# Optimization experiments

Hardware: AMD Instinct MI355X
Metric: run time of the kernel (lower is better)

The kernel has to match this reference:

```python
import jax, jax.numpy as jnp
import numpy as np

N_NODES = 50000
NEG_SLOPE = 0.2


def gat_conv(x, W, att_src, att_dst, b, src, dst, n):
    # x: [N, F_in], W: [F_in, H*C], att_*: [H, C], b: [H*C]
    H, C = att_src.shape
    h = (x @ W).reshape(n, H, C)                       # [N, H, C]
    a_s = (h * att_src).sum(-1)                        # [N, H]
    a_d = (h * att_dst).sum(-1)                        # [N, H]
    e = jax.nn.leaky_relu(a_s[src] + a_d[dst], NEG_SLOPE)  # [E, H]
    # segment softmax over destination node (every node has a self-loop)
    m = jax.ops.segment_max(e, dst, num_segments=n)    # [N, H]
    ex = jnp.exp(e - m[dst])
    denom = jax.ops.segment_sum(ex, dst, num_segments=n)
    alpha = ex / denom[dst]                            # [E, H]
    out = jax.ops.segment_sum(alpha[:, :, None] * h[src], dst, num_segments=n)
    return out.reshape(n, H * C) + b


def setup_inputs() -> dict:
    key = jax.random.key(0)
    ks = jax.random.split(key, 10)
    n, e = N_NODES, 1600000
    x = jax.random.normal(ks[0], (n, 128), dtype=jnp.float32)
    edge_index = jax.random.randint(ks[1], (2, e), 0, n, dtype=jnp.int64)
    s = 0.1
    return {
        "x": x,
        "edge_index": edge_index,
        "W1": jax.random.normal(ks[2], (128, 128), dtype=jnp.float32) * s,
        "att_src1": jax.random.normal(ks[3], (4, 32), dtype=jnp.float32) * s,
        "att_dst1": jax.random.normal(ks[4], (4, 32), dtype=jnp.float32) * s,
        "b1": jnp.zeros((128,), dtype=jnp.float32),
        "W2": jax.random.normal(ks[5], (128, 128), dtype=jnp.float32) * s,
        "att_src2": jax.random.normal(ks[6], (4, 32), dtype=jnp.float32) * s,
        "att_dst2": jax.random.normal(ks[7], (4, 32), dtype=jnp.float32) * s,
        "b2": jnp.zeros((128,), dtype=jnp.float32),
    }


def reference(x, edge_index, W1, att_src1, att_dst1, b1, W2, att_src2, att_dst2, b2):
    n = x.shape[0]
    loops = jnp.arange(n, dtype=edge_index.dtype)
    src = jnp.concatenate([edge_index[0], loops])  # add self-loops (PyG default)
    dst = jnp.concatenate([edge_index[1], loops])
    h = gat_conv(x, W1, att_src1, att_dst1, b1, src, dst, n)
    h = jax.nn.relu(h)
    h = gat_conv(h, W2, att_src2, att_dst2, b2, src, dst, n)
    return (h, h)
```

## Files before the change

kernel.cpp:

```cpp
#include <hip/hip_runtime.h>
#include <hip/hip_bf16.h>
#include <hip/hip_fp16.h>


#define FDIM 128
#define NHEAD 4
#define NB 512

typedef __attribute__((ext_vector_type(16))) float f32x16;
typedef __attribute__((ext_vector_type(8)))  short s16x8;

__device__ inline unsigned short f2bf(float f) {
    union { float f; unsigned u; } v; v.f = f;
    unsigned r = v.u + 0x7fff + ((v.u >> 16) & 1);
    return (unsigned short)(r >> 16);
}
__device__ inline float2 bf2f(unsigned v) {
    union { unsigned u; float f; } a, b;
    a.u = v << 16;
    b.u = v & 0xffff0000u;
    return make_float2(a.f, b.f);
}
__device__ inline void splitbf(float f, short* hi, short* lo) {
    unsigned u = __float_as_uint(f);
    float rem = f - __uint_as_float(u & 0xffff0000u);
    *hi = (short)(u >> 16);
    *lo = (short)(__float_as_uint(rem) >> 16);
}

__global__ __launch_bounds__(256) void prep_hist(const float* __restrict__ W1,
                                                 short* __restrict__ B1hi,
                                                 short* __restrict__ B1lo,
                                                 const float* __restrict__ W2,
                                                 short* __restrict__ B2hi,
                                                 short* __restrict__ B2lo,
                                                 const int* __restrict__ dst, int E,
                                                 unsigned long long magic,
                                                 int* __restrict__ bcnt) {
    __shared__ int sh[NB];
    const int t = threadIdx.x;
    const int b = blockIdx.x;
    if (b < 128) {
        const float* W = (b < 64) ? W1 : W2;
        short* Bhi = (b < 64) ? B1hi : B2hi;
        short* Blo = (b < 64) ? B1lo : B2lo;
        int e = (b & 63) * 256 + t;
        int k = e >> 7, n = e & 127;
        short hi, lo;
        splitbf(W[e], &hi, &lo);
        int idx = n * 128 + (((k >> 3) ^ (n & 15)) << 3) + (k & 7);
        Bhi[idx] = hi;
        Blo[idx] = lo;
        return;
    }
    for (int i = t; i < NB; i += 256) sh[i] = 0;
    __syncthreads();
    const int stride = (gridDim.x - 128) * 256;
    for (int i = (b - 128) * 256 + t; i < E; i += stride) {
        int bk = (int)(((unsigned long long)(unsigned)dst[i] * magic) >> 40);
        atomicAdd(&sh[bk], 1);
    }
    __syncthreads();
    for (int i = t; i < NB; i += 256)
        if (sh[i]) atomicAdd(&bcnt[i], sh[i]);
}

__global__ __launch_bounds__(256) void gemm_mfma(const float* __restrict__ A,
                                                 const short* __restrict__ Bghi,
                                                 const short* __restrict__ Bglo,
                                                 unsigned short* __restrict__ H0,
                                                 unsigned short* __restrict__ H1,
                                                 const float* __restrict__ att_s,
                                                 const float* __restrict__ att_d,
                                                 float* __restrict__ a_s,
                                                 float* __restrict__ a_d, int M) {
    __shared__ short Bsm[2][16384];
    __shared__ float attsm[256];
    const int t = threadIdx.x;
    const int bm = blockIdx.x * 64;

    if (t < 128) attsm[t] = att_s[t];
    else         attsm[t] = att_d[t - 128];

    {
        const uint4* ghi = (const uint4*)Bghi;
        const uint4* glo = (const uint4*)Bglo;
        uint4* shi = (uint4*)&Bsm[0][0];
        uint4* slo = (uint4*)&Bsm[1][0];
        #pragma unroll
        for (int i = 0; i < 8; i++) {
            shi[t + i * 256] = ghi[t + i * 256];
            slo[t + i * 256] = glo[t + i * 256];
        }
    }

    const int lane = t & 63;
    const int w = t >> 6;
    const int wr = w >> 1, wc = w & 1;
    const int m  = lane & 31, h2 = lane >> 5;
    const int grow = bm + wr * 32 + m;

    s16x8 ahi[8], alo[8];
    {
        const bool ok = grow < M;
        const float* ap = A + (size_t)grow * 128 + 8 * h2;
        #pragma unroll
        for (int c = 0; c < 8; c++) {
            float ff[8];
            if (ok) {
                float4 f0 = *(const float4*)(ap + c * 16);
                float4 f1 = *(const float4*)(ap + c * 16 + 4);
                ff[0]=f0.x; ff[1]=f0.y; ff[2]=f0.z; ff[3]=f0.w;
                ff[4]=f1.x; ff[5]=f1.y; ff[6]=f1.z; ff[7]=f1.w;
            } else {
                #pragma unroll
                for (int j = 0; j < 8; j++) ff[j] = 0.f;
            }
            #pragma unroll
            for (int j = 0; j < 8; j++) {
                short hi, lo;
                splitbf(ff[j], &hi, &lo);
                ahi[c][j] = hi;
                alo[c][j] = lo;
            }
        }
    }
    __syncthreads();

    f32x16 acc[2];
    #pragma unroll
    for (int i = 0; i < 16; i++) { acc[0][i] = 0.f; acc[1][i] = 0.f; }

    #pragma unroll
    for (int ni = 0; ni < 2; ni++) {
        const int n = ni * 64 + wc * 32 + m;
        const int nbase = n * 128;
        #pragma unroll
        for (int c = 0; c < 8; c++) {
            int chunk8 = 2 * c + h2;
            int koff = ((chunk8 ^ (n & 15)) << 3);
            s16x8 bhi = *(const s16x8*)&Bsm[0][nbase + koff];
            s16x8 blo = *(const s16x8*)&Bsm[1][nbase + koff];
            acc[ni] = __builtin_amdgcn_mfma_f32_32x32x16_bf16(ahi[c], bhi, acc[ni], 0, 0, 0);
            acc[ni] = __builtin_amdgcn_mfma_f32_32x32x16_bf16(alo[c], bhi, acc[ni], 0, 0, 0);
            acc[ni] = __builtin_amdgcn_mfma_f32_32x32x16_bf16(ahi[c], blo, acc[ni], 0, 0, 0);
        }
    }

    __syncthreads();
    unsigned short* htile = (unsigned short*)&Bsm[0][0];
    #pragma unroll
    for (int ni = 0; ni < 2; ni++) {
        const int colg = ni * 64 + wc * 32 + m;
        #pragma unroll
        for (int r = 0; r < 16; r++) {
            int row = wr * 32 + (r & 3) + 8 * (r >> 2) + 4 * h2;
            htile[row * 128 + colg] = (short)f2bf(acc[ni][r]);
        }
    }
    __syncthreads();

    {
        const int r = t >> 2, q = t & 3;
        const int growr = bm + r;
        if (growr < M) {
            uint4 v0 = *(uint4*)&htile[r * 128 + q * 32];
            uint4 v1 = *(uint4*)&htile[r * 128 + q * 32 + 8];
            uint4 v2 = *(uint4*)&htile[r * 128 + q * 32 + 16];
            uint4 v3 = *(uint4*)&htile[r * 128 + q * 32 + 24];
            unsigned short* Hp = (q < 2) ? H0 : H1;
            uint4* hg = (uint4*)(Hp + (size_t)growr * 64);
            const int qq = q & 1;
            hg[qq * 4 + 0] = v0; hg[qq * 4 + 1] = v1;
            hg[qq * 4 + 2] = v2; hg[qq * 4 + 3] = v3;
            unsigned uu[16] = {v0.x, v0.y, v0.z, v0.w, v1.x, v1.y, v1.z, v1.w,
                               v2.x, v2.y, v2.z, v2.w, v3.x, v3.y, v3.z, v3.w};
            float ps = 0.f, pd = 0.f;
            #pragma unroll
            for (int i = 0; i < 16; i++) {
                float2 f = bf2f(uu[i]);
                ps += f.x * attsm[q * 32 + 2 * i]       + f.y * attsm[q * 32 + 2 * i + 1];
                pd += f.x * attsm[128 + q * 32 + 2 * i] + f.y * attsm[128 + q * 32 + 2 * i + 1];
            }
            a_s[growr * NHEAD + q] = ps;
            a_d[growr * NHEAD + q] = pd;
        }
    }
}

__global__ __launch_bounds__(256) void bucket_scan(const int* __restrict__ bcnt,
                                                   int* __restrict__ bbase,
                                                   int* __restrict__ bcursor,
                                                   int* __restrict__ row_ptr,
                                                   int N, int E) {
    __shared__ int wsum[4];
    const int t = threadIdx.x, lane = t & 63, wid = t >> 6;
    int v0 = bcnt[2 * t], v1 = bcnt[2 * t + 1];
    int s = v0 + v1, incl = s;
    #pragma unroll
    for (int o = 1; o < 64; o <<= 1) {
        int u = __shfl_up(incl, o, 64);
        if (lane >= o) incl += u;
    }
    if (lane == 63) wsum[wid] = incl;
    __syncthreads();
    if (t == 0) {
        int a = 0;
        #pragma unroll
        for (int i = 0; i < 4; i++) { int x = wsum[i]; wsum[i] = a; a += x; }
    }
    __syncthreads();
    int excl = wsum[wid] + incl - s;
    bbase[2 * t] = excl;          bcursor[2 * t] = excl;
    bbase[2 * t + 1] = excl + v0; bcursor[2 * t + 1] = excl + v0;
    if (t == 0) { bbase[NB] = E; row_ptr[N] = E; }
}

__global__ __launch_bounds__(256) void partition(const int* __restrict__ src,
                                                 const int* __restrict__ dst, int E,
                                                 unsigned long long magic,
                                                 int* __restrict__ bcursor,
                                                 int2* __restrict__ ebuf) {
    __shared__ int shc[NB];
    __shared__ int shb[NB];
    __shared__ int shcur[NB];
    const int t = threadIdx.x;
    for (int i = t; i < NB; i += 256) shc[i] = 0;
    __syncthreads();
    const int e0 = blockIdx.x * 4096;
    int myb[16], mys[16], myd[16];
    #pragma unroll
    for (int u = 0; u < 16; u++) {
        int i = e0 + u * 256 + t;
        if (i < E) {
            mys[u] = src[i];
            myd[u] = dst[i];
            int b = (int)(((unsigned long long)(unsigned)myd[u] * magic) >> 40);
            myb[u] = b;
            atomicAdd(&shc[b], 1);
        } else myb[u] = -1;
    }
    __syncthreads();
    for (int i = t; i < NB; i += 256) {
        int c = shc[i];
        shcur[i] = 0;
        if (c) shb[i] = atomicAdd(&bcursor[i], c);
    }
    __syncthreads();
    #pragma unroll
    for (int u = 0; u < 16; u++) {
        if (myb[u] >= 0) {
            int o = atomicAdd(&shcur[myb[u]], 1);
            ebuf[shb[myb[u]] + o] = make_int2(mys[u], myd[u]);
        }
    }
}

__global__ __launch_bounds__(256) void build_bucket(const int2* __restrict__ ebuf,
                                                    const int* __restrict__ bbase,
                                                    int npb, int N,
                                                    int* __restrict__ row_ptr,
                                                    int* __restrict__ col,
                                                    int* __restrict__ edst) {
    __shared__ int degl[256];
    __shared__ int curl[256];
    const int b = blockIdx.x;
    const int t = threadIdx.x, lane = t & 63, wid = t >> 6;
    const int base = bbase[b];
    const int cnt = bbase[b + 1] - base;
    const int node0 = b * npb;
    for (int i = t; i < npb; i += 256) degl[i] = 0;
    __syncthreads();
    for (int i = t; i < cnt; i += 256) {
        int d = ebuf[base + i].y;
        atomicAdd(&degl[d - node0], 1);
    }
    __syncthreads();
    if (wid == 0) {
        int run = 0;
        for (int c = 0; c * 64 < npb; c++) {
            int idx = c * 64 + lane;
            int v = (idx < npb) ? degl[idx] : 0;
            int incl = v;
            #pragma unroll
            for (int o = 1; o < 64; o <<= 1) {
                int u = __shfl_up(incl, o, 64);
                if (lane >= o) incl += u;
            }
            int excl = incl - v + run;
            if (idx < npb) {
                curl[idx] = excl;
                int node = node0 + idx;
                if (node < N) row_ptr[node] = base + excl;
            }
            run += __shfl(incl, 63, 64);
        }
    }
    __syncthreads();
    for (int i = t; i < cnt; i += 256) {
        int2 ed = ebuf[base + i];
        int p = atomicAdd(&curl[ed.y - node0], 1);
        col[base + p] = ed.x;
        edst[base + p] = ed.y;
    }
}

__global__ __launch_bounds__(256) void edge_w(const int* __restrict__ col,
                                              const int* __restrict__ edst,
                                              const float4* __restrict__ as4,
                                              const float4* __restrict__ ad4,
                                              int E,
                                              __half2* __restrict__ w0,
                                              __half2* __restrict__ w1) {
    int i = blockIdx.x * 256 + threadIdx.x;
    if (i >= E) return;
    float4 a = as4[col[i]];
    float4 b = ad4[edst[i]];
    float ex = a.x + b.x, ey = a.y + b.y, ez = a.z + b.z, ew = a.w + b.w;
    ex = fmaxf(ex, 0.2f * ex); ey = fmaxf(ey, 0.2f * ey);
    ez = fmaxf(ez, 0.2f * ez); ew = fmaxf(ew, 0.2f * ew);
    w0[i] = __floats2half2_rn(__expf(ex), __expf(ey));
    w1[i] = __floats2half2_rn(__expf(ez), __expf(ew));
}

__global__ __launch_bounds__(64) void aggregate(const unsigned* __restrict__ h0,
                                                const unsigned* __restrict__ h1,
                                                const __half2* __restrict__ w0,
                                                const __half2* __restrict__ w1,
                                                const float* __restrict__ a_s,
                                                const float* __restrict__ a_d,
                                                const int* __restrict__ row_ptr,
                                                const int* __restrict__ col,
                                                const float* __restrict__ bias,
                                                float* __restrict__ out,
                                                float* __restrict__ out2,
                                                int n, int do_relu) {
    const int b = blockIdx.x;
    const int p = b & 1;
    const unsigned* __restrict__ hp = p ? h1 : h0;
    const __half2* __restrict__ wp = p ? w1 : w0;
    const int t = threadIdx.x;
    const int g = t >> 5;
    const int li = t & 31;
    const int node = (b >> 1) * 2 + g;
    if (node >= n) return;
    const int hd = p * 2 + (li >> 4);
    const bool hiH = (li >> 4) != 0;

    float e = a_s[node * NHEAD + hd] + a_d[node * NHEAD + hd];
    e = fmaxf(e, 0.2f * e);
    float den = __expf(e);
    float2 hv = bf2f(hp[(size_t)node * 32 + li]);
    float num0 = den * hv.x, num1 = den * hv.y;

    const int beg = row_ptr[node], end = row_ptr[node + 1];
    int j = beg;
    for (; j + 8 <= end; j += 8) {
        int s[8];
        #pragma unroll
        for (int u = 0; u < 8; u++) s[u] = col[j + u];
        unsigned v[8]; __half2 hw[8];
        #pragma unroll
        for (int u = 0; u < 8; u++) v[u] = hp[(size_t)s[u] * 32 + li];
        #pragma unroll
        for (int u = 0; u < 8; u++) hw[u] = wp[j + u];
        #pragma unroll
        for (int u = 0; u < 8; u++) {
            float wgt = hiH ? __high2float(hw[u]) : __low2float(hw[u]);
            den += wgt;
            float2 f = bf2f(v[u]);
            num0 += wgt * f.x;
            num1 += wgt * f.y;
        }
    }
    for (; j < end; j++) {
        int s = col[j];
        __half2 hw = wp[j];
        float wgt = hiH ? __high2float(hw) : __low2float(hw);
        den += wgt;
        float2 f = bf2f(hp[(size_t)s * 32 + li]);
        num0 += wgt * f.x;
        num1 += wgt * f.y;
    }
    float2 bv = ((const float2*)bias)[p * 32 + li];
    float rd = 1.0f / den;
    float o0 = num0 * rd + bv.x;
    float o1 = num1 * rd + bv.y;
    if (do_relu) { o0 = fmaxf(o0, 0.f); o1 = fmaxf(o1, 0.f); }
    ((float2*)out)[(size_t)node * 64 + p * 32 + li] = make_float2(o0, o1);
    if (out2) ((float2*)out2)[(size_t)node * 64 + p * 32 + li] = make_float2(o0, o1);
}

extern "C" void kernel_launch(void* const* d_in, const int* in_sizes, int n_in,
                              void* d_out, int out_size, void* d_ws, size_t ws_size,
                              hipStream_t stream) {
    const float* x        = (const float*)d_in[0];
    const int*   edge     = (const int*)d_in[1];
    const float* W1       = (const float*)d_in[2];
    const float* att_s1   = (const float*)d_in[3];
    const float* att_d1   = (const float*)d_in[4];
    const float* b1       = (const float*)d_in[5];
    const float* W2       = (const float*)d_in[6];
    const float* att_s2   = (const float*)d_in[7];
    const float* att_d2   = (const float*)d_in[8];
    const float* b2       = (const float*)d_in[9];
    float* out = (float*)d_out;

    const int N = in_sizes[0] / FDIM;
    const int E = in_sizes[1] / 2;
    const int* src = edge;
    const int* dst = edge + E;

    const int npb = (N + NB - 1) / NB;
    const unsigned long long magic = ((1ull << 40) / (unsigned long long)npb) + 1;

    char* w = (char*)d_ws;
    size_t off = 0;
    auto alloc = [&](size_t bytes) { void* p = w + off; off = (off + bytes + 255) & ~(size_t)255; return p; };
    int*   row_ptr = (int*)alloc((size_t)(N + 1) * 4);
    int*   col     = (int*)alloc((size_t)E * 4);
    int*   edst    = (int*)alloc((size_t)E * 4);
    __half2* w0    = (__half2*)alloc((size_t)E * 4);
    __half2* w1    = (__half2*)alloc((size_t)E * 4);
    int*   bcnt    = (int*)alloc((size_t)NB * 4);
    int*   bbase   = (int*)alloc((size_t)(NB + 1) * 4);
    int*   bcursor = (int*)alloc((size_t)NB * 4);
    unsigned short* h0 = (unsigned short*)alloc((size_t)N * 64 * 2);
    unsigned short* h1 = (unsigned short*)alloc((size_t)N * 64 * 2);
    float* hx      = (float*)alloc((size_t)N * FDIM * 4);
    float* as1     = (float*)alloc((size_t)N * NHEAD * 4);
    float* ad1     = (float*)alloc((size_t)N * NHEAD * 4);
    float* as2     = (float*)alloc((size_t)N * NHEAD * 4);
    float* ad2     = (float*)alloc((size_t)N * NHEAD * 4);
    short* Bg1hi   = (short*)alloc((size_t)128 * 128 * 2);
    short* Bg1lo   = (short*)alloc((size_t)128 * 128 * 2);
    short* Bg2hi   = (short*)alloc((size_t)128 * 128 * 2);
    short* Bg2lo   = (short*)alloc((size_t)128 * 128 * 2);
    int2*  ebuf    = (int2*)hx;
    (void)ws_size;

    hipMemsetAsync(bcnt, 0, (size_t)NB * 4, stream);
    prep_hist<<<128 + 1024, 256, 0, stream>>>(W1, Bg1hi, Bg1lo, W2, Bg2hi, Bg2lo,
                                              dst, E, magic, bcnt);
    bucket_scan<<<1, 256, 0, stream>>>(bcnt, bbase, bcursor, row_ptr, N, E);
    partition<<<(E + 4095) / 4096, 256, 0, stream>>>(src, dst, E, magic, bcursor, ebuf);
    build_bucket<<<NB, 256, 0, stream>>>(ebuf, bbase, npb, N, row_ptr, col, edst);

    const int gblocks = (N + 63) / 64;
    const int eb = (E + 255) / 256;
    const int ablocks = ((N + 1) / 2) * 2;

    gemm_mfma<<<gblocks, 256, 0, stream>>>(x, Bg1hi, Bg1lo, h0, h1,
                                           att_s1, att_d1, as1, ad1, N);
    edge_w<<<eb, 256, 0, stream>>>(col, edst, (const float4*)as1, (const float4*)ad1,
                                   E, w0, w1);
    aggregate<<<ablocks, 64, 0, stream>>>((const unsigned*)h0, (const unsigned*)h1,
                                          w0, w1, as1, ad1, row_ptr, col, b1,
                                          hx, nullptr, N, 1);

    gemm_mfma<<<gblocks, 256, 0, stream>>>(hx, Bg2hi, Bg2lo, h0, h1,
                                           att_s2, att_d2, as2, ad2, N);
    edge_w<<<eb, 256, 0, stream>>>(col, edst, (const float4*)as2, (const float4*)ad2,
                                   E, w0, w1);
    aggregate<<<ablocks, 64, 0, stream>>>((const unsigned*)h0, (const unsigned*)h1,
                                          w0, w1, as2, ad2, row_ptr, col, b2,
                                          out, out + (size_t)N * FDIM, N, 0);
}
```

Before: 336.4 us.

## Split each node's edge list across four lane groups with prefetch and shuffle reduction

The aggregation kernel now gives each node a full 64-lane wavefront. Sixteen lanes cover one half-feature slice using 8-byte loads, and four groups of lanes take interleaved edges. Neighbor indices and weights for the next block of 16 edges are prefetched, and partial sums are combined with cross-group shuffles before a float4 store. This aims to shorten the serial per-node edge loop and widen memory accesses. The cost is the shuffle reduction plus padded dummy gathers for nodes whose degree is not a multiple of 16.

Result: slower. 345.6 us (+2.7%).

```diff
diff --git a/kernel.cpp b/kernel.cpp
--- a/kernel.cpp
+++ b/kernel.cpp
@@ -323,72 +323,109 @@
     w1[i] = __floats2half2_rn(__expf(ez), __expf(ew));
 }
 
-__global__ __launch_bounds__(64) void aggregate(const unsigned* __restrict__ h0,
-                                                const unsigned* __restrict__ h1,
-                                                const __half2* __restrict__ w0,
-                                                const __half2* __restrict__ w1,
-                                                const float* __restrict__ a_s,
-                                                const float* __restrict__ a_d,
-                                                const int* __restrict__ row_ptr,
-                                                const int* __restrict__ col,
-                                                const float* __restrict__ bias,
-                                                float* __restrict__ out,
-                                                float* __restrict__ out2,
-                                                int n, int do_relu) {
+__global__ __launch_bounds__(256) void aggregate(const unsigned* __restrict__ h0,
+                                                 const unsigned* __restrict__ h1,
+                                                 const __half2* __restrict__ w0,
+                                                 const __half2* __restrict__ w1,
+                                                 const float* __restrict__ a_s,
+                                                 const float* __restrict__ a_d,
+                                                 const int* __restrict__ row_ptr,
+                                                 const int* __restrict__ col,
+                                                 const float* __restrict__ bias,
+                                                 float* __restrict__ out,
+                                                 float* __restrict__ out2,
+                                                 int n, int do_relu) {
     const int b = blockIdx.x;
     const int p = b & 1;
     const unsigned* __restrict__ hp = p ? h1 : h0;
     const __half2* __restrict__ wp = p ? w1 : w0;
     const int t = threadIdx.x;
-    const int g = t >> 5;
-    const int li = t & 31;
-    const int node = (b >> 1) * 2 + g;
+    const int node = (b >> 1) * 4 + (t >> 6);
     if (node >= n) return;
-    const int hd = p * 2 + (li >> 4);
-    const bool hiH = (li >> 4) != 0;
-
-    float e = a_s[node * NHEAD + hd] + a_d[node * NHEAD + hd];
-    e = fmaxf(e, 0.2f * e);
-    float den = __expf(e);
-    float2 hv = bf2f(hp[(size_t)node * 32 + li]);
-    float num0 = den * hv.x, num1 = den * hv.y;
+    const int lane = t & 63;
+    const int g  = lane >> 4;
+    const int li = lane & 15;
+    const int hd = p * 2 + (li >> 3);
+    const bool hiH = (li >> 3) != 0;
+
+    float den = 0.f;
+    float nx0 = 0.f, ny0 = 0.f, nx1 = 0.f, ny1 = 0.f;
+    if (g == 0) {
+        float e = a_s[node * NHEAD + hd] + a_d[node * NHEAD + hd];
+        e = fmaxf(e, 0.2f * e);
+        den = __expf(e);
+        uint2 hv = *(const uint2*)&hp[(size_t)node * 32 + 2 * li];
+        float2 f0 = bf2f(hv.x), f1 = bf2f(hv.y);
+        nx0 = den * f0.x; ny0 = den * f0.y;
+        nx1 = den * f1.x; ny1 = den * f1.y;
+    }
 
     const int beg = row_ptr[node], end = row_ptr[node + 1];
-    int j = beg;
-    for (; j + 8 <= end; j += 8) {
-        int s[8];
-        #pragma unroll
-        for (int u = 0; u < 8; u++) s[u] = col[j + u];
-        unsigned v[8]; __half2 hw[8];
-        #pragma unroll
-        for (int u = 0; u < 8; u++) v[u] = hp[(size_t)s[u] * 32 + li];
-        #pragma unroll
-        for (int u = 0; u < 8; u++) hw[u] = wp[j + u];
-        #pragma unroll
-        for (int u = 0; u < 8; u++) {
-            float wgt = hiH ? __high2float(hw[u]) : __low2float(hw[u]);
+    const int nblk = (end - beg + 15) >> 4;
+
+    int cs[4]; unsigned cw[4];
+    #pragma unroll
+    for (int u = 0; u < 4; u++) {
+        int id = beg + u * 4 + g;
+        bool v = id < end;
+        cs[u] = v ? col[id] : node;
+        cw[u] = v ? *(const unsigned*)&wp[id] : 0u;
+    }
+
+    for (int blk = 0; blk < nblk; blk++) {
+        int ns[4]; unsigned nw[4];
+        const bool more = (blk + 1) < nblk;
+        if (more) {
+            int nbase = beg + (blk + 1) * 16;
+            #pragma unroll
+            for (int u = 0; u < 4; u++) {
+                int id = nbase + u * 4 + g;
+                bool v = id < end;
+                ns[u] = v ? col[id] : node;
+                nw[u] = v ? *(const unsigned*)&wp[id] : 0u;
+            }
+        }
+        uint2 hv[4];
+        #pragma unroll
+        for (int u = 0; u < 4; u++)
+            hv[u] = *(const uint2*)&hp[(size_t)cs[u] * 32 + 2 * li];
+        #pragma unroll
+        for (int u = 0; u < 4; u++) {
+            __half2 h2 = *(__half2*)&cw[u];
+            float wgt = hiH ? __high2float(h2) : __low2float(h2);
             den += wgt;
-            float2 f = bf2f(v[u]);
-            num0 += wgt * f.x;
-            num1 += wgt * f.y;
-        }
-    }
-    for (; j < end; j++) {
-        int s = col[j];
-        __half2 hw = wp[j];
-        float wgt = hiH ? __high2float(hw) : __low2float(hw);
-        den += wgt;
-        float2 f = bf2f(hp[(size_t)s * 32 + li]);
-        num0 += wgt * f.x;
-        num1 += wgt * f.y;
-    }
-    float2 bv = ((const float2*)bias)[p * 32 + li];
-    float rd = 1.0f / den;
-    float o0 = num0 * rd + bv.x;
-    float o1 = num1 * rd + bv.y;
-    if (do_relu) { o0 = fmaxf(o0, 0.f); o1 = fmaxf(o1, 0.f); }
-    ((float2*)out)[(size_t)node * 64 + p * 32 + li] = make_float2(o0, o1);
-    if (out2) ((float2*)out2)[(size_t)node * 64 + p * 32 + li] = make_float2(o0, o1);
+            float2 f0 = bf2f(hv[u].x), f1 = bf2f(hv[u].y);
+            nx0 += wgt * f0.x; ny0 += wgt * f0.y;
+            nx1 += wgt * f1.x; ny1 += wgt * f1.y;
+        }
+        if (more) {
+            #pragma unroll
+            for (int u = 0; u < 4; u++) { cs[u] = ns[u]; cw[u] = nw[u]; }
+        }
+    }
+
+    #pragma unroll
+    for (int off = 16; off < 64; off <<= 1) {
+        den += __shfl_xor(den, off, 64);
+        nx0 += __shfl_xor(nx0, off, 64);
+        ny0 += __shfl_xor(ny0, off, 64);
+        nx1 += __shfl_xor(nx1, off, 64);
+        ny1 += __shfl_xor(ny1, off, 64);
+    }
+
+    if (g == 0) {
+        float4 bv = ((const float4*)bias)[p * 16 + li];
+        float rd = 1.0f / den;
+        float4 o;
+        o.x = nx0 * rd + bv.x; o.y = ny0 * rd + bv.y;
+        o.z = nx1 * rd + bv.z; o.w = ny1 * rd + bv.w;
+        if (do_relu) {
+            o.x = fmaxf(o.x, 0.f); o.y = fmaxf(o.y, 0.f);
+            o.z = fmaxf(o.z, 0.f); o.w = fmaxf(o.w, 0.f);
+        }
+        ((float4*)out)[(size_t)node * 32 + p * 16 + li] = o;
+        if (out2) ((float4*)out2)[(size_t)node * 32 + p * 16 + li] = o;
+    }
 }
 
 extern "C" void kernel_launch(void* const* d_in, const int* in_sizes, int n_in,
@@ -448,21 +485,21 @@
 
     const int gblocks = (N + 63) / 64;
     const int eb = (E + 255) / 256;
-    const int ablocks = ((N + 1) / 2) * 2;
+    const int ablocks = ((N + 3) / 4) * 2;
 
     gemm_mfma<<<gblocks, 256, 0, stream>>>(x, Bg1hi, Bg1lo, h0, h1,
                                            att_s1, att_d1, as1, ad1, N);
     edge_w<<<eb, 256, 0, stream>>>(col, edst, (const float4*)as1, (const float4*)ad1,
                                    E, w0, w1);
-    aggregate<<<ablocks, 64, 0, stream>>>((const unsigned*)h0, (const unsigned*)h1,
-                                          w0, w1, as1, ad1, row_ptr, col, b1,
-                                          hx, nullptr, N, 1);
+    aggregate<<<ablocks, 256, 0, stream>>>((const unsigned*)h0, (const unsigned*)h1,
+                                           w0, w1, as1, ad1, row_ptr, col, b1,
+                                           hx, nullptr, N, 1);
 
     gemm_mfma<<<gblocks, 256, 0, stream>>>(hx, Bg2hi, Bg2lo, h0, h1,
                                            att_s2, att_d2, as2, ad2, N);
     edge_w<<<eb, 256, 0, stream>>>(col, edst, (const float4*)as2, (const float4*)ad2,
                                    E, w0, w1);
-    aggregate<<<ablocks, 64, 0, stream>>>((const unsigned*)h0, (const unsigned*)h1,
-                                          w0, w1, as2, ad2, row_ptr, col, b2,
-                                          out, out + (size_t)N * FDIM, N, 0);
-}
+    aggregate<<<ablocks, 256, 0, stream>>>((const unsigned*)h0, (const unsigned*)h1,
+                                           w0, w1, as2, ad2, row_ptr, col, b2,
+                                           out, out + (size_t)N * FDIM, N, 0);
+}
```

## Split features and edge weights into per-head planes for aggregation

Applied to the files above, without the earlier changes.

The bf16 feature matrix and fp16 edge weights are reorganised from two-head halves into four per-head planes. The aggregate kernel now assigns each block to one head, with 16 lanes per node and 4 nodes per block, so each gathered row segment is 64 bytes and each edge weight is a single half. Streaming loads and stores (col, weights, outputs) are marked nontemporal to reduce cache pollution. In exchange, the col and row_ptr traffic doubles because there are four head passes instead of two, and each gather segment is smaller, which could lower gather efficiency.

Result: slower. 426.4 us (+26.7%).

```diff
diff --git a/kernel.cpp b/kernel.cpp
--- a/kernel.cpp
+++ b/kernel.cpp
@@ -68,8 +68,7 @@
 __global__ __launch_bounds__(256) void gemm_mfma(const float* __restrict__ A,
                                                  const short* __restrict__ Bghi,
                                                  const short* __restrict__ Bglo,
-                                                 unsigned short* __restrict__ H0,
-                                                 unsigned short* __restrict__ H1,
+                                                 unsigned short* __restrict__ H,
                                                  const float* __restrict__ att_s,
                                                  const float* __restrict__ att_d,
                                                  float* __restrict__ a_s,
@@ -168,11 +167,8 @@
             uint4 v1 = *(uint4*)&htile[r * 128 + q * 32 + 8];
             uint4 v2 = *(uint4*)&htile[r * 128 + q * 32 + 16];
             uint4 v3 = *(uint4*)&htile[r * 128 + q * 32 + 24];
-            unsigned short* Hp = (q < 2) ? H0 : H1;
-            uint4* hg = (uint4*)(Hp + (size_t)growr * 64);
-            const int qq = q & 1;
-            hg[qq * 4 + 0] = v0; hg[qq * 4 + 1] = v1;
-            hg[qq * 4 + 2] = v2; hg[qq * 4 + 3] = v3;
+            uint4* hg = (uint4*)(H + ((size_t)q * M + growr) * 32);
+            hg[0] = v0; hg[1] = v1; hg[2] = v2; hg[3] = v3;
             unsigned uu[16] = {v0.x, v0.y, v0.z, v0.w, v1.x, v1.y, v1.z, v1.w,
                                v2.x, v2.y, v2.z, v2.w, v3.x, v3.y, v3.z, v3.w};
             float ps = 0.f, pd = 0.f;
@@ -310,8 +306,10 @@
                                               const float4* __restrict__ as4,
                                               const float4* __restrict__ ad4,
                                               int E,
-                                              __half2* __restrict__ w0,
-                                              __half2* __restrict__ w1) {
+                                              unsigned short* __restrict__ q0,
+                                              unsigned short* __restrict__ q1,
+                                              unsigned short* __restrict__ q2,
+                                              unsigned short* __restrict__ q3) {
     int i = blockIdx.x * 256 + threadIdx.x;
     if (i >= E) return;
     float4 a = as4[col[i]];
@@ -319,14 +317,18 @@
     float ex = a.x + b.x, ey = a.y + b.y, ez = a.z + b.z, ew = a.w + b.w;
     ex = fmaxf(ex, 0.2f * ex); ey = fmaxf(ey, 0.2f * ey);
     ez = fmaxf(ez, 0.2f * ez); ew = fmaxf(ew, 0.2f * ew);
-    w0[i] = __floats2half2_rn(__expf(ex), __expf(ey));
-    w1[i] = __floats2half2_rn(__expf(ez), __expf(ew));
-}
-
-__global__ __launch_bounds__(64) void aggregate(const unsigned* __restrict__ h0,
-                                                const unsigned* __restrict__ h1,
-                                                const __half2* __restrict__ w0,
-                                                const __half2* __restrict__ w1,
+    __half hx = __float2half(__expf(ex));
+    __half hy = __float2half(__expf(ey));
+    __half hz = __float2half(__expf(ez));
+    __half hw = __float2half(__expf(ew));
+    q0[i] = *(unsigned short*)&hx;
+    q1[i] = *(unsigned short*)&hy;
+    q2[i] = *(unsigned short*)&hz;
+    q3[i] = *(unsigned short*)&hw;
+}
+
+__global__ __launch_bounds__(64) void aggregate(const unsigned short* __restrict__ hq,
+                                                const unsigned short* __restrict__ wq,
                                                 const float* __restrict__ a_s,
                                                 const float* __restrict__ a_d,
                                                 const int* __restrict__ row_ptr,
@@ -334,39 +336,45 @@
                                                 const float* __restrict__ bias,
                                                 float* __restrict__ out,
                                                 float* __restrict__ out2,
-                                                int n, int do_relu) {
+                                                int n, int E, int do_relu) {
     const int b = blockIdx.x;
-    const int p = b & 1;
-    const unsigned* __restrict__ hp = p ? h1 : h0;
-    const __half2* __restrict__ wp = p ? w1 : w0;
+    const int p = b & 3;
+    const unsigned* __restrict__ hp =
+        (const unsigned*)(hq + (size_t)p * n * 32);
+    const unsigned short* __restrict__ wp = wq + (size_t)p * E;
     const int t = threadIdx.x;
-    const int g = t >> 5;
-    const int li = t & 31;
-    const int node = (b >> 1) * 2 + g;
-    if (node >= n) return;
-    const int hd = p * 2 + (li >> 4);
-    const bool hiH = (li >> 4) != 0;
-
-    float e = a_s[node * NHEAD + hd] + a_d[node * NHEAD + hd];
+    const int g  = t >> 4;
+    const int li = t & 15;
+    const int node = (b >> 2) * 4 + g;
+    const bool valid = node < n;
+    const int nd = valid ? node : 0;
+
+    float e = a_s[nd * NHEAD + p] + a_d[nd * NHEAD + p];
     e = fmaxf(e, 0.2f * e);
     float den = __expf(e);
-    float2 hv = bf2f(hp[(size_t)node * 32 + li]);
-    float num0 = den * hv.x, num1 = den * hv.y;
-
-    const int beg = row_ptr[node], end = row_ptr[node + 1];
+    float num0, num1;
+    {
+        float2 hv = bf2f(hp[(size_t)nd * 16 + li]);
+        num0 = den * hv.x;
+        num1 = den * hv.y;
+    }
+
+    const int beg = row_ptr[nd];
+    const int end = valid ? row_ptr[nd + 1] : beg;
     int j = beg;
     for (; j + 8 <= end; j += 8) {
         int s[8];
         #pragma unroll
-        for (int u = 0; u < 8; u++) s[u] = col[j + u];
-        unsigned v[8]; __half2 hw[8];
-        #pragma unroll
-        for (int u = 0; u < 8; u++) v[u] = hp[(size_t)s[u] * 32 + li];
-        #pragma unroll
-        for (int u = 0; u < 8; u++) hw[u] = wp[j + u];
+        for (int u = 0; u < 8; u++) s[u] = __builtin_nontemporal_load(&col[j + u]);
+        unsigned v[8];
+        #pragma unroll
+        for (int u = 0; u < 8; u++) v[u] = hp[(size_t)s[u] * 16 + li];
+        unsigned short hw[8];
+        #pragma unroll
+        for (int u = 0; u < 8; u++) hw[u] = __builtin_nontemporal_load(&wp[j + u]);
         #pragma unroll
         for (int u = 0; u < 8; u++) {
-            float wgt = hiH ? __high2float(hw[u]) : __low2float(hw[u]);
+            float wgt = __half2float(*(const __half*)&hw[u]);
             den += wgt;
             float2 f = bf2f(v[u]);
             num0 += wgt * f.x;
@@ -375,20 +383,27 @@
     }
     for (; j < end; j++) {
         int s = col[j];
-        __half2 hw = wp[j];
-        float wgt = hiH ? __high2float(hw) : __low2float(hw);
+        unsigned short hw = wp[j];
+        float wgt = __half2float(*(const __half*)&hw);
         den += wgt;
-        float2 f = bf2f(hp[(size_t)s * 32 + li]);
+        float2 f = bf2f(hp[(size_t)s * 16 + li]);
         num0 += wgt * f.x;
         num1 += wgt * f.y;
     }
-    float2 bv = ((const float2*)bias)[p * 32 + li];
-    float rd = 1.0f / den;
-    float o0 = num0 * rd + bv.x;
-    float o1 = num1 * rd + bv.y;
-    if (do_relu) { o0 = fmaxf(o0, 0.f); o1 = fmaxf(o1, 0.f); }
-    ((float2*)out)[(size_t)node * 64 + p * 32 + li] = make_float2(o0, o1);
-    if (out2) ((float2*)out2)[(size_t)node * 64 + p * 32 + li] = make_float2(o0, o1);
+
+    if (valid) {
+        float2 bv = ((const float2*)bias)[p * 16 + li];
+        float rd = 1.0f / den;
+        float o0 = num0 * rd + bv.x;
+        float o1 = num1 * rd + bv.y;
+        if (do_relu) { o0 = fmaxf(o0, 0.f); o1 = fmaxf(o1, 0.f); }
+        float2 o = make_float2(o0, o1);
+        double dv;
+        __builtin_memcpy(&dv, &o, 8);
+        __builtin_nontemporal_store(dv, (double*)((float2*)out + (size_t)node * 64 + p * 16 + li));
+        if (out2)
+            __builtin_nontemporal_store(dv, (double*)((float2*)out2 + (size_t)node * 64 + p * 16 + li));
+    }
 }
 
 extern "C" void kernel_launch(void* const* d_in, const int* in_sizes, int n_in,
@@ -420,13 +435,11 @@
     int*   row_ptr = (int*)alloc((size_t)(N + 1) * 4);
     int*   col     = (int*)alloc((size_t)E * 4);
     int*   edst    = (int*)alloc((size_t)E * 4);
-    __half2* w0    = (__half2*)alloc((size_t)E * 4);
-    __half2* w1    = (__half2*)alloc((size_t)E * 4);
+    unsigned short* wqa = (unsigned short*)alloc((size_t)4 * E * 2);
     int*   bcnt    = (int*)alloc((size_t)NB * 4);
     int*   bbase   = (int*)alloc((size_t)(NB + 1) * 4);
     int*   bcursor = (int*)alloc((size_t)NB * 4);
-    unsigned short* h0 = (unsigned short*)alloc((size_t)N * 64 * 2);
-    unsigned short* h1 = (unsigned short*)alloc((size_t)N * 64 * 2);
+    unsigned short* h = (unsigned short*)alloc((size_t)4 * N * 32 * 2);
     float* hx      = (float*)alloc((size_t)N * FDIM * 4);
     float* as1     = (float*)alloc((size_t)N * NHEAD * 4);
     float* ad1     = (float*)alloc((size_t)N * NHEAD * 4);
@@ -448,21 +461,21 @@
 
     const int gblocks = (N + 63) / 64;
     const int eb = (E + 255) / 256;
-    const int ablocks = ((N + 1) / 2) * 2;
-
-    gemm_mfma<<<gblocks, 256, 0, stream>>>(x, Bg1hi, Bg1lo, h0, h1,
+    const int ablocks = ((N + 3) / 4) * 4;
+
+    gemm_mfma<<<gblocks, 256, 0, stream>>>(x, Bg1hi, Bg1lo, h,
                                            att_s1, att_d1, as1, ad1, N);
     edge_w<<<eb, 256, 0, stream>>>(col, edst, (const float4*)as1, (const float4*)ad1,
-                                   E, w0, w1);
-    aggregate<<<ablocks, 64, 0, stream>>>((const unsigned*)h0, (const unsigned*)h1,
-                                          w0, w1, as1, ad1, row_ptr, col, b1,
-                                          hx, nullptr, N, 1);
-
-    gemm_mfma<<<gblocks, 256, 0, stream>>>(hx, Bg2hi, Bg2lo, h0, h1,
+                                   E, wqa, wqa + (size_t)E, wqa + (size_t)2 * E,
+                                   wqa + (size_t)3 * E);
+    aggregate<<<ablocks, 64, 0, stream>>>(h, wqa, as1, ad1, row_ptr, col, b1,
+                                          hx, nullptr, N, E, 1);
+
+    gemm_mfma<<<gblocks, 256, 0, stream>>>(hx, Bg2hi, Bg2lo, h,
                                            att_s2, att_d2, as2, ad2, N);
     edge_w<<<eb, 256, 0, stream>>>(col, edst, (const float4*)as2, (const float4*)ad2,
-                                   E, w0, w1);
-    aggregate<<<ablocks, 64, 0, stream>>>((const unsigned*)h0, (const unsigned*)h1,
-                                          w0, w1, as2, ad2, row_ptr, col, b2,
-                                          out, out + (size_t)N * FDIM, N, 0);
-}
+                                   E, wqa, wqa + (size_t)E, wqa + (size_t)2 * E,
+                                   wqa + (size_t)3 * E);
+    aggregate<<<ablocks, 64, 0, stream>>>(h, wqa, as2, ad2, row_ptr, col, b2,
+                                          out, out + (size_t)N * FDIM, N, E, 0);
+}
```

## Fuse edge attention weights into aggregate and store scores head-major

Applied to the files above, without the earlier changes.

Removes the separate edge_w kernel and the per-edge fp16 weight arrays and destination index array. The aggregate kernel now gathers the source attention score per edge and computes leaky-relu and exp inline. The a_s/a_d score arrays are switched to head-major layout so each half-wave gathers from a contiguous per-head array. This saves two edge-sized passes and their global writes and reads, at the cost of an extra random gather and an exp per edge inside aggregate. The gemm kernel must use M as the row count for the new layout.

Result: faster. 327.8 us (-2.6%).

```diff
diff --git a/kernel.cpp b/kernel.cpp
--- a/kernel.cpp
+++ b/kernel.cpp
@@ -182,8 +182,8 @@
                 ps += f.x * attsm[q * 32 + 2 * i]       + f.y * attsm[q * 32 + 2 * i + 1];
                 pd += f.x * attsm[128 + q * 32 + 2 * i] + f.y * attsm[128 + q * 32 + 2 * i + 1];
             }
-            a_s[growr * NHEAD + q] = ps;
-            a_d[growr * NHEAD + q] = pd;
+            a_s[(size_t)q * M + growr] = ps;
+            a_d[(size_t)q * M + growr] = pd;
         }
     }
 }
@@ -260,8 +260,7 @@
                                                     const int* __restrict__ bbase,
                                                     int npb, int N,
                                                     int* __restrict__ row_ptr,
-                                                    int* __restrict__ col,
-                                                    int* __restrict__ edst) {
+                                                    int* __restrict__ col) {
     __shared__ int degl[256];
     __shared__ int curl[256];
     const int b = blockIdx.x;
@@ -301,32 +300,11 @@
         int2 ed = ebuf[base + i];
         int p = atomicAdd(&curl[ed.y - node0], 1);
         col[base + p] = ed.x;
-        edst[base + p] = ed.y;
-    }
-}
-
-__global__ __launch_bounds__(256) void edge_w(const int* __restrict__ col,
-                                              const int* __restrict__ edst,
-                                              const float4* __restrict__ as4,
-                                              const float4* __restrict__ ad4,
-                                              int E,
-                                              __half2* __restrict__ w0,
-                                              __half2* __restrict__ w1) {
-    int i = blockIdx.x * 256 + threadIdx.x;
-    if (i >= E) return;
-    float4 a = as4[col[i]];
-    float4 b = ad4[edst[i]];
-    float ex = a.x + b.x, ey = a.y + b.y, ez = a.z + b.z, ew = a.w + b.w;
-    ex = fmaxf(ex, 0.2f * ex); ey = fmaxf(ey, 0.2f * ey);
-    ez = fmaxf(ez, 0.2f * ez); ew = fmaxf(ew, 0.2f * ew);
-    w0[i] = __floats2half2_rn(__expf(ex), __expf(ey));
-    w1[i] = __floats2half2_rn(__expf(ez), __expf(ew));
+    }
 }
 
 __global__ __launch_bounds__(64) void aggregate(const unsigned* __restrict__ h0,
                                                 const unsigned* __restrict__ h1,
-                                                const __half2* __restrict__ w0,
-                                                const __half2* __restrict__ w1,
                                                 const float* __restrict__ a_s,
                                                 const float* __restrict__ a_d,
                                                 const int* __restrict__ row_ptr,
@@ -338,16 +316,16 @@
     const int b = blockIdx.x;
     const int p = b & 1;
     const unsigned* __restrict__ hp = p ? h1 : h0;
-    const __half2* __restrict__ wp = p ? w1 : w0;
     const int t = threadIdx.x;
     const int g = t >> 5;
     const int li = t & 31;
     const int node = (b >> 1) * 2 + g;
     if (node >= n) return;
     const int hd = p * 2 + (li >> 4);
-    const bool hiH = (li >> 4) != 0;
-
-    float e = a_s[node * NHEAD + hd] + a_d[node * NHEAD + hd];
+    const float* __restrict__ as_h = a_s + (size_t)hd * n;
+    const float adv = a_d[(size_t)hd * n + node];
+
+    float e = as_h[node] + adv;
     e = fmaxf(e, 0.2f * e);
     float den = __expf(e);
     float2 hv = bf2f(hp[(size_t)node * 32 + li]);
@@ -359,14 +337,17 @@
         int s[8];
         #pragma unroll
         for (int u = 0; u < 8; u++) s[u] = col[j + u];
-        unsigned v[8]; __half2 hw[8];
+        unsigned v[8];
         #pragma unroll
         for (int u = 0; u < 8; u++) v[u] = hp[(size_t)s[u] * 32 + li];
-        #pragma unroll
-        for (int u = 0; u < 8; u++) hw[u] = wp[j + u];
+        float av[8];
+        #pragma unroll
+        for (int u = 0; u < 8; u++) av[u] = as_h[s[u]];
         #pragma unroll
         for (int u = 0; u < 8; u++) {
-            float wgt = hiH ? __high2float(hw[u]) : __low2float(hw[u]);
+            float ee = av[u] + adv;
+            ee = fmaxf(ee, 0.2f * ee);
+            float wgt = __expf(ee);
             den += wgt;
             float2 f = bf2f(v[u]);
             num0 += wgt * f.x;
@@ -375,8 +356,9 @@
     }
     for (; j < end; j++) {
         int s = col[j];
-        __half2 hw = wp[j];
-        float wgt = hiH ? __high2float(hw) : __low2float(hw);
+        float ee = as_h[s] + adv;
+        ee = fmaxf(ee, 0.2f * ee);
+        float wgt = __expf(ee);
         den += wgt;
         float2 f = bf2f(hp[(size_t)s * 32 + li]);
         num0 += wgt * f.x;
@@ -419,19 +401,16 @@
     auto alloc = [&](size_t bytes) { void* p = w + off; off = (off + bytes + 255) & ~(size_t)255; return p; };
     int*   row_ptr = (int*)alloc((size_t)(N + 1) * 4);
     int*   col     = (int*)alloc((size_t)E * 4);
-    int*   edst    = (int*)alloc((size_t)E * 4);
-    __half2* w0    = (__half2*)alloc((size_t)E * 4);
-    __half2* w1    = (__half2*)alloc((size_t)E * 4);
     int*   bcnt    = (int*)alloc((size_t)NB * 4);
     int*   bbase   = (int*)alloc((size_t)(NB + 1) * 4);
     int*   bcursor = (int*)alloc((size_t)NB * 4);
     unsigned short* h0 = (unsigned short*)alloc((size_t)N * 64 * 2);
     unsigned short* h1 = (unsigned short*)alloc((size_t)N * 64 * 2);
     float* hx      = (float*)alloc((size_t)N * FDIM * 4);
-    float* as1     = (float*)alloc((size_t)N * NHEAD * 4);
-    float* ad1     = (float*)alloc((size_t)N * NHEAD * 4);
-    float* as2     = (float*)alloc((size_t)N * NHEAD * 4);
-    float* ad2     = (float*)alloc((size_t)N * NHEAD * 4);
+    float* as1     = (float*)alloc((size_t)NHEAD * N * 4);
+    float* ad1     = (float*)alloc((size_t)NHEAD * N * 4);
+    float* as2     = (float*)alloc((size_t)NHEAD * N * 4);
+    float* ad2     = (float*)alloc((size_t)NHEAD * N * 4);
     short* Bg1hi   = (short*)alloc((size_t)128 * 128 * 2);
     short* Bg1lo   = (short*)alloc((size_t)128 * 128 * 2);
     short* Bg2hi   = (short*)alloc((size_t)128 * 128 * 2);
@@ -444,25 +423,20 @@
                                               dst, E, magic, bcnt);
     bucket_scan<<<1, 256, 0, stream>>>(bcnt, bbase, bcursor, row_ptr, N, E);
     partition<<<(E + 4095) / 4096, 256, 0, stream>>>(src, dst, E, magic, bcursor, ebuf);
-    build_bucket<<<NB, 256, 0, stream>>>(ebuf, bbase, npb, N, row_ptr, col, edst);
+    build_bucket<<<NB, 256, 0, stream>>>(ebuf, bbase, npb, N, row_ptr, col);
 
     const int gblocks = (N + 63) / 64;
-    const int eb = (E + 255) / 256;
     const int ablocks = ((N + 1) / 2) * 2;
 
     gemm_mfma<<<gblocks, 256, 0, stream>>>(x, Bg1hi, Bg1lo, h0, h1,
                                            att_s1, att_d1, as1, ad1, N);
-    edge_w<<<eb, 256, 0, stream>>>(col, edst, (const float4*)as1, (const float4*)ad1,
-                                   E, w0, w1);
     aggregate<<<ablocks, 64, 0, stream>>>((const unsigned*)h0, (const unsigned*)h1,
-                                          w0, w1, as1, ad1, row_ptr, col, b1,
+                                          as1, ad1, row_ptr, col, b1,
                                           hx, nullptr, N, 1);
 
     gemm_mfma<<<gblocks, 256, 0, stream>>>(hx, Bg2hi, Bg2lo, h0, h1,
                                            att_s2, att_d2, as2, ad2, N);
-    edge_w<<<eb, 256, 0, stream>>>(col, edst, (const float4*)as2, (const float4*)ad2,
-                                   E, w0, w1);
     aggregate<<<ablocks, 64, 0, stream>>>((const unsigned*)h0, (const unsigned*)h1,
-                                          w0, w1, as2, ad2, row_ptr, col, b2,
+                                          as2, ad2, row_ptr, col, b2,
                                           out, out + (size_t)N * FDIM, N, 0);
 }
```
